# Performance work log

Measured on AMD Instinct MI355X. Metric: run time of the kernel, lower is better.

## Reference

```python
import jax, jax.numpy as jnp
import numpy as np
from jax import lax

WIN = 11
SIGMA = 1.5
C1 = 0.01 ** 2  # L = 1 (inputs in [0,1], matches pytorch_msssim dynamic-range inference)
C2 = 0.03 ** 2
WEIGHTS = np.array([0.0448, 0.2856, 0.3001, 0.2363, 0.1333], dtype=np.float32)


def _gauss_window(channels, dtype):
    x = np.arange(WIN, dtype=np.float64) - WIN // 2
    g = np.exp(-(x ** 2) / (2.0 * SIGMA ** 2))
    g = g / g.sum()
    w2d = np.outer(g, g).astype(np.float32)          # (11,11)
    w = np.broadcast_to(w2d, (channels, 1, WIN, WIN))  # depthwise OIHW
    return jnp.asarray(w, dtype=dtype)


def _dwconv(x, w):
    # depthwise valid conv, NCHW
    return lax.conv_general_dilated(
        x, w, window_strides=(1, 1), padding='VALID',
        dimension_numbers=('NCHW', 'OIHW', 'NCHW'),
        feature_group_count=x.shape[1])


def _ssim(img1, img2, w):
    mu1 = _dwconv(img1, w)
    mu2 = _dwconv(img2, w)
    mu1_sq, mu2_sq, mu1_mu2 = mu1 * mu1, mu2 * mu2, mu1 * mu2
    sigma1_sq = _dwconv(img1 * img1, w) - mu1_sq
    sigma2_sq = _dwconv(img2 * img2, w) - mu2_sq
    sigma12 = _dwconv(img1 * img2, w) - mu1_mu2
    v1 = 2.0 * sigma12 + C2
    v2 = sigma1_sq + sigma2_sq + C2
    cs = jnp.mean(v1 / v2)
    ssim_map = ((2.0 * mu1_mu2 + C1) * v1) / ((mu1_sq + mu2_sq + C1) * v2)
    return jnp.mean(ssim_map), cs


def _avgpool2(x):
    B, C, H, W = x.shape
    return x.reshape(B, C, H // 2, 2, W // 2, 2).mean(axis=(3, 5))


def _msssim(img1, img2):
    w = _gauss_window(img1.shape[1], img1.dtype)
    weights = jnp.asarray(WEIGHTS, dtype=img1.dtype)
    mssim, mcs = [], []
    for _ in range(len(WEIGHTS)):  # 5 fixed pyramid levels
        s, c = _ssim(img1, img2, w)
        mssim.append(s)
        mcs.append(c)
        img1, img2 = _avgpool2(img1), _avgpool2(img2)
    mssim = jnp.stack(mssim)
    mcs = jnp.stack(mcs)
    pow1 = mcs ** weights
    pow2 = mssim ** weights
    # literal translation of pytorch_msssim: torch.prod(pow1[:-1] * pow2[-1])
    return jnp.prod(pow1[:-1] * pow2[-1])


def setup_inputs() -> dict:
    key = jax.random.key(0)
    k1, k2 = jax.random.split(key)
    shape = (16, 3, 512, 512)
    reconst = jax.random.uniform(k1, shape, dtype=jnp.float32)
    original = jax.random.uniform(k2, shape, dtype=jnp.float32)
    return {"reconst": reconst, "original": original}


def reference(reconst, original):
    msssim = _msssim(original, reconst)
    mse = jnp.mean((original - reconst) ** 2)
    loss = mse - msssim + 1.0
    return (loss, msssim)
```

## Files before the change

### kernel.cpp

```cpp
#include <hip/hip_runtime.h>
#include <math.h>


#define NPLANES 48

struct GaussW { float g[11]; };

typedef float v2f __attribute__((ext_vector_type(2)));

#define PYR2_OFF  4177920
#define P_L0      8355840
#define P_L1      8358912
#define P_L2      8360448
#define P_L3      8361216
#define P_L4      8361408
#define P_MSE     8361480

#define C1F 1.0e-4f
#define C2F 9.0e-4f

__global__ __launch_bounds__(256, 4) void ssim_l0(
    const float* __restrict__ x1, const float* __restrict__ x2, GaussW gw,
    float* __restrict__ partials, float* __restrict__ msep,
    float* __restrict__ d1, float* __restrict__ d2)
{
  constexpr int W = 512, Ho = 502, BH = 32, WB = 256, STRIDE = WB + 12;
  constexpr int W2 = 256;

  __shared__ v2f vbuf[4][STRIDE];
  __shared__ float red[3][4];

  const int tid = threadIdx.x;
  const int col = tid;
  const int bx = blockIdx.x, by = blockIdx.y, bz = blockIdx.z;
  const int gcol = bx * WB + col;
  const int plane = bz;
  const size_t pb = (size_t)plane * W * W;
  const float* q1 = x1 + pb + gcol;
  const float* q2 = x2 + pb + gcol;
  const int gr0 = BH * by;
  const int ROWS = ((W - gr0) < (BH + 10)) ? (W - gr0) : (BH + 10);
  const bool xtra = (bx * WB + WB + col) < W;

  float f1[11], f2[11], f3[11], f4[11];
#pragma unroll
  for (int j = 0; j < 11; ++j) { f1[j] = 0.f; f2[j] = 0.f; f3[j] = 0.f; f4[j] = 0.f; }

  float mse_acc = 0.f, ssim_acc = 0.f, cs_acc = 0.f;

#define LOADR(R, a, b, ae, be)                                          \
  {                                                                     \
    size_t ro = (size_t)(gr0 + (R)) * W;                                \
    a = q1[ro]; b = q2[ro];                                             \
    ae = 0.f; be = 0.f;                                                 \
    if (col < 12 && xtra) { ae = q1[ro + WB]; be = q2[ro + WB]; }       \
    if ((R) < BH) {                                                     \
      float d_ = a - b;                                                 \
      mse_acc = fmaf(d_, d_, mse_acc);                                  \
    }                                                                   \
  }

#define STAGE(R, a, b, ae, be)                                          \
  {                                                                     \
    const int sl_ = (R) & 3;                                            \
    vbuf[sl_][col] = (v2f){a, b};                                       \
    if (col < 12) vbuf[sl_][WB + col] = (v2f){ae, be};                  \
  }

#define PROW(R)                                                         \
  {                                                                     \
    const v2f* r_ = &vbuf[(R) & 3][col];                                \
    float s1 = 0.f, s2 = 0.f, s3 = 0.f, s4 = 0.f;                       \
    _Pragma("unroll") for (int k = 0; k < 11; ++k) {                    \
      v2f ab = r_[k];                                                   \
      float av = ab.x, bv = ab.y, w = gw.g[k];                          \
      float wa = w * av, wb = w * bv;                                   \
      s1 += wa; s2 += wb;                                               \
      s3 = fmaf(wa, bv, s3);                                            \
      s4 = fmaf(wa, av, s4);                                            \
      s4 = fmaf(wb, bv, s4);                                            \
    }                                                                   \
    _Pragma("unroll") for (int j = 10; j >= 1; --j) {                   \
      f1[j] = fmaf(gw.g[j], s1, f1[j - 1]);                             \
      f2[j] = fmaf(gw.g[j], s2, f2[j - 1]);                             \
      f3[j] = fmaf(gw.g[j], s3, f3[j - 1]);                             \
      f4[j] = fmaf(gw.g[j], s4, f4[j - 1]);                             \
    }                                                                   \
    f1[0] = gw.g[0] * s1;                                               \
    f2[0] = gw.g[0] * s2;                                               \
    f3[0] = gw.g[0] * s3;                                               \
    f4[0] = gw.g[0] * s4;                                               \
    if ((R) >= 10 && gcol < Ho) {                                       \
      float m1 = f1[10], m2 = f2[10], e12 = f3[10], esq = f4[10];       \
      float m12 = m1 * m2;                                              \
      float msq = fmaf(m1, m1, m2 * m2);                                \
      float v1 = 2.f * (e12 - m12) + C2F;                               \
      float vv2 = (esq - msq) + C2F;                                    \
      float csv = v1 * __builtin_amdgcn_rcpf(vv2);                      \
      cs_acc += csv;                                                    \
      ssim_acc += csv * (2.f * m12 + C1F) *                             \
                  __builtin_amdgcn_rcpf(msq + C1F);                     \
    }                                                                   \
  }

  {
    float a0, b0, ae0, be0, a1, b1, ae1, be1;
    LOADR(0, a0, b0, ae0, be0)
    LOADR(1, a1, b1, ae1, be1)
    STAGE(0, a0, b0, ae0, be0)
    STAGE(1, a1, b1, ae1, be1)
  }
  __syncthreads();

  for (int i = 0; i < ROWS / 2; ++i) {
    const int r0 = 2 * i, r1 = 2 * i + 1;
    const bool have = (r0 + 2) < ROWS;

    float na0 = 0.f, nb0 = 0.f, nae0 = 0.f, nbe0 = 0.f;
    float na1 = 0.f, nb1 = 0.f, nae1 = 0.f, nbe1 = 0.f;
    if (have) {
      LOADR(r0 + 2, na0, nb0, nae0, nbe0)
      LOADR(r1 + 2, na1, nb1, nae1, nbe1)
    }

    PROW(r0)
    PROW(r1)

    if (r0 < BH && col < (WB / 2)) {
      v2f x0 = vbuf[r0 & 3][2 * col], x1v = vbuf[r0 & 3][2 * col + 1];
      v2f y0 = vbuf[r1 & 3][2 * col], y1v = vbuf[r1 & 3][2 * col + 1];
      int orow = (gr0 >> 1) + i;
      size_t ob = (size_t)plane * W2 * W2 + (size_t)orow * W2 + bx * (WB / 2) + col;
      d1[ob] = 0.25f * ((x0.x + x1v.x) + (y0.x + y1v.x));
      d2[ob] = 0.25f * ((x0.y + x1v.y) + (y0.y + y1v.y));
    }

    if (have) {
      STAGE(r0 + 2, na0, nb0, nae0, nbe0)
      STAGE(r1 + 2, na1, nb1, nae1, nbe1)
      __syncthreads();
    }
  }
#undef LOADR
#undef STAGE
#undef PROW

#pragma unroll
  for (int off = 32; off; off >>= 1) {
    ssim_acc += __shfl_down(ssim_acc, off);
    cs_acc += __shfl_down(cs_acc, off);
    mse_acc += __shfl_down(mse_acc, off);
  }
  int wave = tid >> 6, lane = tid & 63;
  if (lane == 0) {
    red[0][wave] = ssim_acc;
    red[1][wave] = cs_acc;
    red[2][wave] = mse_acc;
  }
  __syncthreads();
  if (tid == 0) {
    float s = 0.f, cc = 0.f, m = 0.f;
#pragma unroll
    for (int i = 0; i < 4; ++i) { s += red[0][i]; cc += red[1][i]; m += red[2][i]; }
    int bi = (bz * gridDim.y + by) * gridDim.x + bx;
    partials[2 * bi] = s;
    partials[2 * bi + 1] = cc;
    msep[bi] = m;
  }
}

template <int LOGW, int BH, int PP>
__device__ __forceinline__ void ssim_level(
    char* ldsraw, float (*red)[4], int by, int bz,
    const float* __restrict__ x1, const float* __restrict__ x2,
    const GaussW& gw, float* __restrict__ partials, int bi)
{
  constexpr int W = 1 << LOGW;
  constexpr int Ho = W - 10;
  constexpr int WB = W;
  constexpr int P = 256 / WB;
  constexpr int STRIDE = WB + 12;
  constexpr int S = 1 << PP;
  constexpr float INV = 1.f / (float)(S * S);

  typedef v2f Slot[P][STRIDE];
  Slot* vbuf = (Slot*)ldsraw;

  const int tid = threadIdx.x;
  const int p = tid >> LOGW;
  const int col = tid & (WB - 1);
  const int plane = bz * P + p;
  const int gr0 = BH * by;
  const int ROWS = ((W - gr0) < (BH + 10)) ? (W - gr0) : (BH + 10);

  const float* q1 = x1 + (size_t)plane * 65536;
  const float* q2 = x2 + (size_t)plane * 65536;

  float acc0[11], acc1[11], acc2[11], acc3[11], acc4[11];
#pragma unroll
  for (int j = 0; j < 11; ++j) {
    acc0[j] = 0.f; acc1[j] = 0.f; acc2[j] = 0.f; acc3[j] = 0.f; acc4[j] = 0.f;
  }

  float ssim_acc = 0.f, cs_acc = 0.f;

#define LOADV(R, a, b)                                                  \
  {                                                                     \
    const float* pa = q1 + (size_t)((gr0 + (R)) << PP) * 256 + (col << PP); \
    const float* pb = q2 + (size_t)((gr0 + (R)) << PP) * 256 + (col << PP); \
    float sa = 0.f, sb = 0.f;                                           \
    _Pragma("unroll 1") for (int i_ = 0; i_ < S; ++i_) {                \
      _Pragma("unroll") for (int j_ = 0; j_ < S; ++j_) {                \
        sa += pa[i_ * 256 + j_];                                        \
        sb += pb[i_ * 256 + j_];                                        \
      }                                                                 \
    }                                                                   \
    a = sa * INV; b = sb * INV;                                         \
  }

  {
    float a, b;
    LOADV(0, a, b)
    vbuf[0][p][col] = (v2f){a, b};
    if (col < 12) vbuf[0][p][WB + col] = (v2f){0.f, 0.f};
  }
  __syncthreads();

  int cur = 0;
  for (int rr = 0; rr < ROWS; ++rr) {
    int nxt = cur + 1; if (nxt == 3) nxt = 0;
    const bool have = (rr + 1) < ROWS;

    float a = 0.f, b = 0.f;
    if (have) LOADV(rr + 1, a, b)

    const v2f* r = &vbuf[cur][p][col];
    float s1 = 0.f, s2 = 0.f, s11 = 0.f, s22 = 0.f, s12 = 0.f;
#pragma unroll
    for (int k = 0; k < 11; ++k) {
      v2f ab = r[k];
      float av = ab.x, bv = ab.y, w = gw.g[k];
      float wa = w * av, wb = w * bv;
      s1 += wa; s2 += wb;
      s11 = fmaf(wa, av, s11);
      s22 = fmaf(wb, bv, s22);
      s12 = fmaf(wa, bv, s12);
    }

#pragma unroll
    for (int j = 10; j >= 1; --j) {
      acc0[j] = fmaf(gw.g[j], s1, acc0[j - 1]);
      acc1[j] = fmaf(gw.g[j], s2, acc1[j - 1]);
      acc2[j] = fmaf(gw.g[j], s11, acc2[j - 1]);
      acc3[j] = fmaf(gw.g[j], s22, acc3[j - 1]);
      acc4[j] = fmaf(gw.g[j], s12, acc4[j - 1]);
    }
    acc0[0] = gw.g[0] * s1;
    acc1[0] = gw.g[0] * s2;
    acc2[0] = gw.g[0] * s11;
    acc3[0] = gw.g[0] * s22;
    acc4[0] = gw.g[0] * s12;

    if (rr >= 10 && col < Ho) {
      float m1 = acc0[10], m2 = acc1[10];
      float m1sq = m1 * m1, m2sq = m2 * m2, m12 = m1 * m2;
      float v1 = 2.f * (acc4[10] - m12) + C2F;
      float v2 = (acc2[10] - m1sq) + (acc3[10] - m2sq) + C2F;
      float csv = v1 * __builtin_amdgcn_rcpf(v2);
      cs_acc += csv;
      ssim_acc += csv * (2.f * m12 + C1F) *
                  __builtin_amdgcn_rcpf(m1sq + m2sq + C1F);
    }

    if (have) {
      vbuf[nxt][p][col] = (v2f){a, b};
      if (col < 12) vbuf[nxt][p][WB + col] = (v2f){0.f, 0.f};
      __syncthreads();
    }
    cur = nxt;
  }
#undef LOADV

#pragma unroll
  for (int off = 32; off; off >>= 1) {
    ssim_acc += __shfl_down(ssim_acc, off);
    cs_acc += __shfl_down(cs_acc, off);
  }
  int wave = tid >> 6, lane = tid & 63;
  if (lane == 0) {
    red[0][wave] = ssim_acc;
    red[1][wave] = cs_acc;
  }
  __syncthreads();
  if (tid == 0) {
    float s = 0.f, cc = 0.f;
#pragma unroll
    for (int i = 0; i < 4; ++i) { s += red[0][i]; cc += red[1][i]; }
    partials[2 * bi] = s;
    partials[2 * bi + 1] = cc;
  }
}

__global__ __launch_bounds__(256, 4) void ssim_rest(
    const float* __restrict__ A1, const float* __restrict__ B1, GaussW gw,
    float* __restrict__ ws)
{
  __shared__ char lds[8448];
  __shared__ float red[2][4];

  const int b = blockIdx.x;
  if (b < 768) {
    ssim_level<8, 16, 0>(lds, red, b & 15, b >> 4, A1, B1, gw, ws + P_L1, b);
  } else if (b < 1152) {
    const int i = b - 768;
    ssim_level<7, 8, 1>(lds, red, i & 15, i >> 4, A1, B1, gw, ws + P_L2, i);
  } else if (b < 1248) {
    const int i = b - 1152;
    ssim_level<6, 8, 2>(lds, red, i & 7, i >> 3, A1, B1, gw, ws + P_L3, i);
  } else {
    const int i = b - 1248;
    ssim_level<5, 4, 3>(lds, red, i % 6, i / 6, A1, B1, gw, ws + P_L4, i);
  }
}

__global__ __launch_bounds__(256) void final_kernel(
    const float* __restrict__ ws, float* __restrict__ out)
{
  __shared__ double sred[2][4];
  __shared__ double fin[11];
  const int tid = threadIdx.x;
  const int offs[5] = {P_L0, P_L1, P_L2, P_L3, P_L4};
  const int cnts[5] = {1536, 768, 384, 96, 36};

  for (int l = 0; l < 5; ++l) {
    double s0 = 0.0, s1 = 0.0;
    for (int i = tid; i < cnts[l]; i += 256) {
      s0 += (double)ws[offs[l] + 2 * i];
      s1 += (double)ws[offs[l] + 2 * i + 1];
    }
#pragma unroll
    for (int off = 32; off; off >>= 1) {
      s0 += __shfl_down(s0, off);
      s1 += __shfl_down(s1, off);
    }
    if ((tid & 63) == 0) { sred[0][tid >> 6] = s0; sred[1][tid >> 6] = s1; }
    __syncthreads();
    if (tid == 0) {
      double aa = 0.0, bb = 0.0;
      for (int i = 0; i < 4; ++i) { aa += sred[0][i]; bb += sred[1][i]; }
      fin[l] = aa;
      fin[5 + l] = bb;
    }
    __syncthreads();
  }

  {
    double s0 = 0.0;
    for (int i = tid; i < 1536; i += 256) s0 += (double)ws[P_MSE + i];
#pragma unroll
    for (int off = 32; off; off >>= 1) s0 += __shfl_down(s0, off);
    if ((tid & 63) == 0) sred[0][tid >> 6] = s0;
    __syncthreads();
    if (tid == 0) {
      double aa = 0.0;
      for (int i = 0; i < 4; ++i) aa += sred[0][i];
      fin[10] = aa;
    }
    __syncthreads();
  }

  if (tid == 0) {
    const double wts[5] = {0.0448, 0.2856, 0.3001, 0.2363, 0.1333};
    const double dims[5] = {502.0, 246.0, 118.0, 54.0, 22.0};
    double mssim[5], mcs[5];
    for (int l = 0; l < 5; ++l) {
      double n = 48.0 * dims[l] * dims[l];
      mssim[l] = fin[l] / n;
      mcs[l] = fin[5 + l] / n;
    }
    double p2last = pow(mssim[4], wts[4]);
    double prod = 1.0;
    for (int i = 0; i < 4; ++i) prod *= pow(mcs[i], wts[i]) * p2last;
    double msssim = prod;
    double mse = fin[10] / 12582912.0;
    out[0] = (float)(mse - msssim + 1.0);
    out[1] = (float)msssim;
  }
}

extern "C" void kernel_launch(void* const* d_in, const int* in_sizes, int n_in,
                              void* d_out, int out_size, void* d_ws, size_t ws_size,
                              hipStream_t stream)
{
  const float* rec = (const float*)d_in[0];
  const float* orig = (const float*)d_in[1];
  float* ws = (float*)d_ws;
  float* out = (float*)d_out;

  GaussW gw;
  {
    double g[11], s = 0.0;
    for (int i = 0; i < 11; ++i) {
      double x = (double)i - 5.0;
      g[i] = exp(-(x * x) / 4.5);
      s += g[i];
    }
    for (int i = 0; i < 11; ++i) gw.g[i] = (float)(g[i] / s);
  }

  float* A1 = ws + 0;
  float* B1 = ws + PYR2_OFF;

  ssim_l0<<<dim3(2, 16, 48), 256, 0, stream>>>(
      orig, rec, gw, ws + P_L0, ws + P_MSE, A1, B1);

  ssim_rest<<<dim3(1284), 256, 0, stream>>>(A1, B1, gw, ws);

  final_kernel<<<dim3(1), dim3(256), 0, stream>>>(ws, out);
}
```

Baseline: 151.4 us.

## Split pyramid levels into per-level kernels emitting pooled next level

Replaces the single merged kernel for levels 1-4, which re-pooled the level-1 images on the fly with strided multi-element loads, with one kernel per level. Each level kernel also writes the 2x2 average-pooled images for the next level from its LDS row buffer. This cuts redundant global reads at the deeper levels. The cost is three extra kernel launches run in series, and the small late levels get very few blocks.

```diff
diff --git a/kernel.cpp b/kernel.cpp
--- a/kernel.cpp
+++ b/kernel.cpp
@@ -169,32 +169,35 @@
   }
 }
 
-template <int LOGW, int BH, int PP>
-__device__ __forceinline__ void ssim_level(
-    char* ldsraw, float (*red)[4], int by, int bz,
-    const float* __restrict__ x1, const float* __restrict__ x2,
-    const GaussW& gw, float* __restrict__ partials, int bi)
+template <int LOGW, int BH, int DO_POOL>
+__global__ __launch_bounds__(256, 4) void ssim_band(
+    const float* __restrict__ x1, const float* __restrict__ x2, GaussW gw,
+    float* __restrict__ partials,
+    float* __restrict__ d1, float* __restrict__ d2)
 {
   constexpr int W = 1 << LOGW;
   constexpr int Ho = W - 10;
-  constexpr int WB = W;
-  constexpr int P = 256 / WB;
+  constexpr int LOGWB = (LOGW > 8) ? 8 : LOGW;
+  constexpr int WB = 1 << LOGWB;
+  constexpr int P = 256 >> LOGWB;
   constexpr int STRIDE = WB + 12;
-  constexpr int S = 1 << PP;
-  constexpr float INV = 1.f / (float)(S * S);
-
-  typedef v2f Slot[P][STRIDE];
-  Slot* vbuf = (Slot*)ldsraw;
+  constexpr int W2 = W >> 1;
+
+  __shared__ v2f vbuf[3][P][STRIDE];
+  __shared__ float red[2][4];
 
   const int tid = threadIdx.x;
-  const int p = tid >> LOGW;
+  const int p = tid >> LOGWB;
   const int col = tid & (WB - 1);
+  const int bx = blockIdx.x, by = blockIdx.y, bz = blockIdx.z;
+  const int gcol = bx * WB + col;
   const int plane = bz * P + p;
+  const size_t pb = (size_t)plane * W * W;
+  const float* q1 = x1 + pb + gcol;
+  const float* q2 = x2 + pb + gcol;
   const int gr0 = BH * by;
   const int ROWS = ((W - gr0) < (BH + 10)) ? (W - gr0) : (BH + 10);
-
-  const float* q1 = x1 + (size_t)plane * 65536;
-  const float* q2 = x2 + (size_t)plane * 65536;
+  const bool xtra = (bx * WB + WB + col) < W;
 
   float acc0[11], acc1[11], acc2[11], acc3[11], acc4[11];
 #pragma unroll
@@ -204,35 +207,28 @@
 
   float ssim_acc = 0.f, cs_acc = 0.f;
 
-#define LOADV(R, a, b)                                                  \
-  {                                                                     \
-    const float* pa = q1 + (size_t)((gr0 + (R)) << PP) * 256 + (col << PP); \
-    const float* pb = q2 + (size_t)((gr0 + (R)) << PP) * 256 + (col << PP); \
-    float sa = 0.f, sb = 0.f;                                           \
-    _Pragma("unroll 1") for (int i_ = 0; i_ < S; ++i_) {                \
-      _Pragma("unroll") for (int j_ = 0; j_ < S; ++j_) {                \
-        sa += pa[i_ * 256 + j_];                                        \
-        sb += pb[i_ * 256 + j_];                                        \
-      }                                                                 \
-    }                                                                   \
-    a = sa * INV; b = sb * INV;                                         \
-  }
-
   {
-    float a, b;
-    LOADV(0, a, b)
+    size_t ro = (size_t)gr0 * W;
+    float a = q1[ro], b = q2[ro];
+    float ae = 0.f, be = 0.f;
+    if (col < 12 && xtra) { ae = q1[ro + WB]; be = q2[ro + WB]; }
     vbuf[0][p][col] = (v2f){a, b};
-    if (col < 12) vbuf[0][p][WB + col] = (v2f){0.f, 0.f};
+    if (col < 12) vbuf[0][p][WB + col] = (v2f){ae, be};
   }
   __syncthreads();
 
   int cur = 0;
   for (int rr = 0; rr < ROWS; ++rr) {
     int nxt = cur + 1; if (nxt == 3) nxt = 0;
+    int prv = cur - 1; if (prv < 0) prv = 2;
     const bool have = (rr + 1) < ROWS;
 
-    float a = 0.f, b = 0.f;
-    if (have) LOADV(rr + 1, a, b)
+    float a = 0.f, b = 0.f, ae = 0.f, be = 0.f;
+    if (have) {
+      size_t ro = (size_t)(gr0 + rr + 1) * W;
+      a = q1[ro]; b = q2[ro];
+      if (col < 12 && xtra) { ae = q1[ro + WB]; be = q2[ro + WB]; }
+    }
 
     const v2f* r = &vbuf[cur][p][col];
     float s1 = 0.f, s2 = 0.f, s11 = 0.f, s22 = 0.f, s12 = 0.f;
@@ -261,7 +257,7 @@
     acc3[0] = gw.g[0] * s22;
     acc4[0] = gw.g[0] * s12;
 
-    if (rr >= 10 && col < Ho) {
+    if (rr >= 10 && gcol < Ho) {
       float m1 = acc0[10], m2 = acc1[10];
       float m1sq = m1 * m1, m2sq = m2 * m2, m12 = m1 * m2;
       float v1 = 2.f * (acc4[10] - m12) + C2F;
@@ -272,14 +268,22 @@
                   __builtin_amdgcn_rcpf(m1sq + m2sq + C1F);
     }
 
+    if (DO_POOL && (rr & 1) && rr < BH && col < (WB / 2)) {
+      v2f x0 = vbuf[prv][p][2 * col], x1v = vbuf[prv][p][2 * col + 1];
+      v2f y0 = vbuf[cur][p][2 * col], y1v = vbuf[cur][p][2 * col + 1];
+      int orow = (gr0 >> 1) + (rr >> 1);
+      size_t ob = (size_t)plane * W2 * W2 + (size_t)orow * W2 + bx * (WB / 2) + col;
+      d1[ob] = 0.25f * ((x0.x + x1v.x) + (y0.x + y1v.x));
+      d2[ob] = 0.25f * ((x0.y + x1v.y) + (y0.y + y1v.y));
+    }
+
     if (have) {
       vbuf[nxt][p][col] = (v2f){a, b};
-      if (col < 12) vbuf[nxt][p][WB + col] = (v2f){0.f, 0.f};
+      if (col < 12) vbuf[nxt][p][WB + col] = (v2f){ae, be};
       __syncthreads();
     }
     cur = nxt;
   }
-#undef LOADV
 
 #pragma unroll
   for (int off = 32; off; off >>= 1) {
@@ -296,30 +300,9 @@
     float s = 0.f, cc = 0.f;
 #pragma unroll
     for (int i = 0; i < 4; ++i) { s += red[0][i]; cc += red[1][i]; }
+    int bi = (bz * gridDim.y + by) * gridDim.x + bx;
     partials[2 * bi] = s;
     partials[2 * bi + 1] = cc;
-  }
-}
-
-__global__ __launch_bounds__(256, 4) void ssim_rest(
-    const float* __restrict__ A1, const float* __restrict__ B1, GaussW gw,
-    float* __restrict__ ws)
-{
-  __shared__ char lds[8448];
-  __shared__ float red[2][4];
-
-  const int b = blockIdx.x;
-  if (b < 768) {
-    ssim_level<8, 16, 0>(lds, red, b & 15, b >> 4, A1, B1, gw, ws + P_L1, b);
-  } else if (b < 1152) {
-    const int i = b - 768;
-    ssim_level<7, 8, 1>(lds, red, i & 15, i >> 4, A1, B1, gw, ws + P_L2, i);
-  } else if (b < 1248) {
-    const int i = b - 1152;
-    ssim_level<6, 8, 2>(lds, red, i & 7, i >> 3, A1, B1, gw, ws + P_L3, i);
-  } else {
-    const int i = b - 1248;
-    ssim_level<5, 4, 3>(lds, red, i % 6, i / 6, A1, B1, gw, ws + P_L4, i);
   }
 }
 
@@ -409,12 +392,25 @@
   }
 
   float* A1 = ws + 0;
+  float* A2 = ws + 3145728;
+  float* A3 = ws + 3932160;
+  float* A4 = ws + 4128768;
   float* B1 = ws + PYR2_OFF;
+  float* B2 = ws + PYR2_OFF + 3145728;
+  float* B3 = ws + PYR2_OFF + 3932160;
+  float* B4 = ws + PYR2_OFF + 4128768;
 
   ssim_l0<<<dim3(2, 16, 48), 256, 0, stream>>>(
       orig, rec, gw, ws + P_L0, ws + P_MSE, A1, B1);
 
-  ssim_rest<<<dim3(1284), 256, 0, stream>>>(A1, B1, gw, ws);
+  ssim_band<8, 16, 1><<<dim3(1, 16, 48), 256, 0, stream>>>(
+      A1, B1, gw, ws + P_L1, A2, B2);
+  ssim_band<7, 8, 1><<<dim3(1, 16, 24), 256, 0, stream>>>(
+      A2, B2, gw, ws + P_L2, A3, B3);
+  ssim_band<6, 8, 1><<<dim3(1, 8, 12), 256, 0, stream>>>(
+      A3, B3, gw, ws + P_L3, A4, B4);
+  ssim_band<5, 4, 0><<<dim3(1, 6, 6), 256, 0, stream>>>(
+      A4, B4, gw, ws + P_L4, nullptr, nullptr);
 
   final_kernel<<<dim3(1), dim3(256), 0, stream>>>(ws, out);
 }
```

After: 145.0 us. -4.2%, faster.
